# Kernel optimization log

Measured on AMD Instinct MI355X. Metric: run time of the kernel, lower is better.

The kernel has to match this reference:

```python
import jax, jax.numpy as jnp
import numpy as np
from jax import lax

HID = 256
ITERS = 8
KT, KH, KW = 3, 7, 7
NBLK = 3
B_, T_, H_, W_, CIN = 1, 8, 32, 32, 128
NQ = 256


def _layernorm(x, scale, bias, eps=1e-6):
    mu = jnp.mean(x, axis=-1, keepdims=True)
    var = jnp.mean(jnp.square(x - mu), axis=-1, keepdims=True)
    return (x - mu) * lax.rsqrt(var + eps) * scale + bias


def _convssm3d(x, A_kernel, B_kernel):
    # x: (B,T,H,W,C); kernels: (C,kt,kh,kw)
    B, T, H, W, C = x.shape
    A_stable = 0.9 * jnp.tanh(A_kernel)
    tt = (jnp.arange(KT) - KT // 2) % T
    th = (jnp.arange(KH) - KH // 2) % H
    tw = (jnp.arange(KW) - KW // 2) % W
    TT, TH, TW = jnp.meshgrid(tt, th, tw, indexing='ij')

    def to_freq(k):
        pad = jnp.zeros((C, T, H, W), x.dtype).at[:, TT, TH, TW].set(k)
        return jnp.fft.fftn(pad, axes=(1, 2, 3)).transpose(1, 2, 3, 0)[None]  # (1,T,H,W,C)

    A_f = to_freq(A_stable)
    B_f = to_freq(B_kernel)
    Bx_f = B_f * jnp.fft.fftn(x, axes=(1, 2, 3))
    shape = (ITERS,) + x.shape
    a_seq = jnp.broadcast_to(A_f, shape)
    b_seq = jnp.broadcast_to(Bx_f, shape)

    def op(left, right):
        return (left[0] * right[0], right[0] * left[1] + right[1])

    _, h_all = lax.associative_scan(op, (a_seq, b_seq), axis=0)
    return jnp.fft.ifftn(h_all[-1], axes=(1, 2, 3)).real


def setup_inputs() -> dict:
    key = jax.random.key(0)
    ks = jax.random.split(key, 10)
    s = 0.02
    return {
        'video_features': jax.random.normal(ks[0], (B_, T_, H_, W_, CIN), jnp.float32),
        'query_points': jax.random.uniform(ks[1], (B_, NQ, 3), jnp.float32),
        'conv_w': jax.random.normal(ks[2], (CIN, HID), jnp.float32) * s,
        'conv_b': jnp.zeros((HID,), jnp.float32),
        'A_kernels': jax.random.normal(ks[3], (NBLK, HID, KT, KH, KW), jnp.float32) * s,
        'B_kernels': jax.random.normal(ks[4], (NBLK, HID, KT, KH, KW), jnp.float32) * s,
        'ln_scale': jnp.ones((NBLK, HID), jnp.float32),
        'ln_bias': jnp.zeros((NBLK, HID), jnp.float32),
        'mlp_w1': jax.random.normal(ks[5], (NBLK, HID, 4 * HID), jnp.float32) * s,
        'mlp_b1': jnp.zeros((NBLK, 4 * HID), jnp.float32),
        'mlp_w2': jax.random.normal(ks[6], (NBLK, 4 * HID, HID), jnp.float32) * s,
        'mlp_b2': jnp.zeros((NBLK, HID), jnp.float32),
        'traj_w': jax.random.normal(ks[7], (HID, 2), jnp.float32) * s,
        'traj_b': jnp.zeros((2,), jnp.float32),
        'occ_w': jax.random.normal(ks[8], (HID, 1), jnp.float32) * s,
        'occ_b': jnp.zeros((1,), jnp.float32),
    }


def reference(video_features, query_points, conv_w, conv_b, A_kernels, B_kernels,
              ln_scale, ln_bias, mlp_w1, mlp_b1, mlp_w2, mlp_b2,
              traj_w, traj_b, occ_w, occ_b):
    # 1x1x1 conv == channel dense. Query scatter in original is a zeros no-op.
    x = jnp.einsum('bthwc,cd->bthwd', video_features, conv_w) + conv_b
    for i in range(NBLK):
        h = _convssm3d(x, A_kernels[i], B_kernels[i])
        h = _layernorm(h, ln_scale[i], ln_bias[i])
        x = x + h
        m = jax.nn.gelu(x @ mlp_w1[i] + mlp_b1[i])  # approximate gelu (flax default)
        x = x + (m @ mlp_w2[i] + mlp_b2[i])
    feat = jnp.mean(x, axis=(2, 3))  # (B,T,C)
    N = query_points.shape[1]
    fe = jnp.broadcast_to(feat[:, None], (feat.shape[0], N) + feat.shape[1:])  # (B,N,T,C)
    trajectories = fe @ traj_w + traj_b + query_points[..., 1:3][:, :, None, :]  # (B,N,T,2)
    occlusion = jax.nn.sigmoid((fe @ occ_w + occ_b)[..., 0])  # (B,N,T)
    return trajectories, occlusion
```

## Files before the change

### kernel.cpp

```cpp
#include <hip/hip_runtime.h>
#include <hip/hip_bf16.h>
#include <math.h>

#define Tn 8
#define Hn 32
#define Wn 32
#define Pn 8192
#define Cn 256
#define CINn 128
#define NTAP 147
#define PADW 40

typedef short s8v __attribute__((ext_vector_type(8)));
typedef float f4v __attribute__((ext_vector_type(4)));
typedef __hip_bfloat16 bf16;

__device__ __forceinline__ float gelu_f(float v) {
    return 0.5f * v * (1.0f + tanhf(0.7978845608028654f * (v + 0.044715f * v * v * v)));
}

__device__ __forceinline__ void gload_lds16(const bf16* g, bf16* l) {
    __builtin_amdgcn_global_load_lds(
        (const __attribute__((address_space(1))) void*)g,
        (__attribute__((address_space(3))) void*)l, 16, 0, 0);
}

__global__ __launch_bounds__(256) void tcast_all_k(
        const float* __restrict__ convw, const float* __restrict__ w1,
        const float* __restrict__ w2, const float* __restrict__ video,
        bf16* __restrict__ cwT, bf16* __restrict__ w1T, bf16* __restrict__ w2T,
        bf16* __restrict__ vb) {
    const int z = blockIdx.z;
    const int tid = (int)threadIdx.x;
    if (z == 7) {
        const int bx = (int)blockIdx.y * 32 + (int)blockIdx.x;
        const int i = bx * 256 + tid;
        const float4 v = ((const float4*)video)[i];
        vb[i * 4 + 0] = __float2bfloat16(v.x);
        vb[i * 4 + 1] = __float2bfloat16(v.y);
        vb[i * 4 + 2] = __float2bfloat16(v.z);
        vb[i * 4 + 3] = __float2bfloat16(v.w);
        return;
    }
    const float* in;
    bf16* out;
    int R, C;
    if (z == 0)      { in = convw;                          out = cwT;                          R = CINn; C = Cn;   }
    else if (z < 4)  { const int i = z - 1;
                       in = w1 + (size_t)i * Cn * 1024;     out = w1T + (size_t)i * 1024 * Cn;  R = Cn;   C = 1024; }
    else             { const int i = z - 4;
                       in = w2 + (size_t)i * 1024 * Cn;     out = w2T + (size_t)i * Cn * 1024;  R = 1024; C = Cn;   }
    if ((int)blockIdx.x >= (C >> 5) || (int)blockIdx.y >= (R >> 5)) return;

    __shared__ float tile[32][33];
    const int tx = tid & 31, ty = tid >> 5;
    const int rb = blockIdx.y << 5, cb = blockIdx.x << 5;
#pragma unroll
    for (int p = 0; p < 4; ++p)
        tile[ty + p * 8][tx] = in[(size_t)(rb + ty + p * 8) * C + cb + tx];
    __syncthreads();
#pragma unroll
    for (int p = 0; p < 4; ++p)
        out[(size_t)(cb + ty + p * 8) * R + rb + tx] = __float2bfloat16(tile[tx][ty + p * 8]);
}

template <int BN, int MODE>
__global__ __launch_bounds__(256) void gemm_bf16_k(
        const bf16* __restrict__ A, const bf16* __restrict__ Wt,
        const float* __restrict__ bias, float* __restrict__ Cf,
        bf16* __restrict__ Cb, bf16* __restrict__ Cpl, int M, int N, int K) {
    constexpr int BM = 128;
    constexpr int NW = BN / 2;
    constexpr int NF = BN / 32;
    constexpr int ALOADS = (BM * 8) / 256;
    constexpr int BLOADS = (BN * 8) / 256;
    __shared__ s8v As[8 * BM];
    __shared__ s8v Bs[8 * BN];

    const int tid = (int)threadIdx.x;
    const int lane = tid & 63, wid = tid >> 6;
    const int wm = wid & 1, wn = wid >> 1;
    const int l15 = lane & 15, l4 = lane >> 4;
    const int m0 = blockIdx.y * BM;
    const int n0 = blockIdx.x * BN;

    f4v acc[4][NF];
#pragma unroll
    for (int i = 0; i < 4; ++i)
#pragma unroll
        for (int j = 0; j < NF; ++j)
#pragma unroll
            for (int r = 0; r < 4; ++r) acc[i][j][r] = 0.f;

    const bf16* Aptr[ALOADS];
#pragma unroll
    for (int j = 0; j < ALOADS; ++j) {
        const int cid = j * 256 + tid;
        Aptr[j] = A + (size_t)(m0 + (cid & (BM - 1))) * K + (cid / BM) * 8;
    }
    const bf16* Bptr[BLOADS];
#pragma unroll
    for (int j = 0; j < BLOADS; ++j) {
        const int cid = j * 256 + tid;
        Bptr[j] = Wt + (size_t)(n0 + (cid & (BN - 1))) * K + (cid / BN) * 8;
    }

    for (int kb = 0; kb < K; kb += 64) {
#pragma unroll
        for (int j = 0; j < ALOADS; ++j)
            gload_lds16(Aptr[j] + kb, (bf16*)&As[j * 256 + tid]);
#pragma unroll
        for (int j = 0; j < BLOADS; ++j)
            gload_lds16(Bptr[j] + kb, (bf16*)&Bs[j * 256 + tid]);
        __syncthreads();

        s8v af[2][4], bfr[2][NF];
#pragma unroll
        for (int ks = 0; ks < 2; ++ks) {
#pragma unroll
            for (int i = 0; i < 4; ++i)
                af[ks][i] = As[(ks * 4 + l4) * BM + wm * 64 + i * 16 + l15];
#pragma unroll
            for (int j = 0; j < NF; ++j)
                bfr[ks][j] = Bs[(ks * 4 + l4) * BN + wn * NW + j * 16 + l15];
        }
#pragma unroll
        for (int ks = 0; ks < 2; ++ks)
#pragma unroll
            for (int i = 0; i < 4; ++i)
#pragma unroll
                for (int j = 0; j < NF; ++j)
                    acc[i][j] = __builtin_amdgcn_mfma_f32_16x16x32_bf16(
                        af[ks][i], bfr[ks][j], acc[i][j], 0, 0, 0);
        __syncthreads();
    }

#pragma unroll
    for (int i = 0; i < 4; ++i) {
        const int rbase = m0 + wm * 64 + i * 16 + l4 * 4;
#pragma unroll
        for (int j = 0; j < NF; ++j) {
            const int col = n0 + wn * NW + j * 16 + l15;
            const float bv = bias[col];
#pragma unroll
            for (int r = 0; r < 4; ++r) {
                const size_t idx = (size_t)(rbase + r) * N + col;
                float v = acc[i][j][r] + bv;
                if (MODE == 0) Cf[idx] = v;
                if (MODE == 1) Cb[idx] = __float2bfloat16(gelu_f(v));
                if (MODE == 2) { v += Cf[idx]; Cf[idx] = v; }
                if (MODE != 1 && Cpl != nullptr)
                    Cpl[(size_t)col * Pn + rbase + r] = __float2bfloat16(v);
            }
        }
    }
}

#define CLOADS(AS, BS0, BS1, body) do {                                       \
    const int bb_ = (body);                                                   \
    const int kt_ = bb_ < 7 ? 0 : (bb_ < 14 ? 1 : 2);                         \
    const int kh_ = bb_ - kt_ * 7;                                            \
    BS0 = *(const s8v*)&tw[bb_][u0][0];                                       \
    BS1 = *(const s8v*)&tw[bb_][u1][0];                                       \
    _Pragma("unroll")                                                         \
    for (int i_ = 0; i_ < 2; ++i_) {                                          \
        const int tp_ = (tout[i_] - kt_ + 9) & 7;                             \
        const int hin_ = (hl[i_] + 35 - kh_) & 31;                            \
        AS[i_] = *(const s8v*)&pl[(tp_ * 32 + hin_) * PADW + aoff];           \
    }                                                                         \
} while (0)

#define CMFMA(AS, BS0, BS1) do {                                              \
    _Pragma("unroll")                                                         \
    for (int i_ = 0; i_ < 2; ++i_) {                                          \
        acc[i_][0] = __builtin_amdgcn_mfma_f32_16x16x32_bf16(AS[i_], BS0, acc[i_][0], 0, 0, 0); \
        acc[i_][1] = __builtin_amdgcn_mfma_f32_16x16x32_bf16(AS[i_], BS1, acc[i_][1], 0, 0, 0); \
    }                                                                         \
} while (0)

__global__ __launch_bounds__(512) void conv_ssm_k(
        const bf16* __restrict__ xplb,
        const float* __restrict__ Ak,
        const float* __restrict__ Bk,
        float* __restrict__ hpo) {
    __shared__ __align__(16) bf16 Pl[2][256 * PADW];
    __shared__ __align__(16) bf16 Tw[2][21][32][8];
    __shared__ float wtap[2][NTAP];

    const int c = blockIdx.x;
    const int tid = (int)threadIdx.x;
    const int lane = tid & 63, wv = tid >> 6;
    const int l15 = lane & 15, l4 = lane >> 4;

    if (tid < NTAP) {
        wtap[0][tid] = Bk[(size_t)c * NTAP + tid];
        wtap[1][tid] = 0.9f * tanhf(Ak[(size_t)c * NTAP + tid]);
    }
    {
        const s8v* src = (const s8v*)(xplb + (size_t)c * Pn);
#pragma unroll
        for (int j = 0; j < 2; ++j) {
            const int g = j * 512 + tid;
            *(s8v*)&Pl[0][(g >> 2) * PADW + (g & 3) * 8] = src[g];
        }
    }
    __syncthreads();
    for (int e = tid; e < 2 * 21 * 32; e += 512) {
        const int sel = e / 672, rem = e % 672;
        const int body = rem >> 5, u = rem & 31;
        const float* tp = &wtap[sel][body * 7];
        bf16 row[8];
#pragma unroll
        for (int j = 0; j < 8; ++j) {
            const int kw = (u - j) & 31;
            row[j] = __float2bfloat16((kw < 7) ? tp[kw] : 0.f);
        }
        *(s8v*)&Tw[sel][body][u][0] = *(const s8v*)row;
    }

    const int u0 = (l15 - l4 * 8 + 3) & 31;
    const int u1 = (l15 + 16 - l4 * 8 + 3) & 31;
    int tout[2], hl[2];
#pragma unroll
    for (int i = 0; i < 2; ++i) {
        const int f = wv * 2 + i;
        tout[i] = f >> 1;
        hl[i] = ((f & 1) << 4) + l15;
    }
    const int aoff = l4 * 8;

    float hsum[16];
#pragma unroll
    for (int i = 0; i < 16; ++i) hsum[i] = 0.f;
    __syncthreads();

#pragma unroll 1
    for (int it = 0; it < 8; ++it) {
        const bf16* pl = Pl[it & 1];
        bf16* pd = Pl[(it + 1) & 1];
        const bf16 (*tw)[32][8] = Tw[(it == 0) ? 0 : 1];

        f4v acc[2][2];
#pragma unroll
        for (int i = 0; i < 2; ++i)
#pragma unroll
            for (int hf = 0; hf < 2; ++hf)
#pragma unroll
                for (int r = 0; r < 4; ++r) acc[i][hf][r] = 0.f;

        s8v a0[2], a1[2], b00, b01, b10, b11;
        CLOADS(a0, b00, b01, 0);
#pragma unroll 1
        for (int b = 0; b < 20; b += 2) {
            CLOADS(a1, b10, b11, b + 1);
            CMFMA(a0, b00, b01);
            CLOADS(a0, b00, b01, b + 2);
            CMFMA(a1, b10, b11);
        }
        CMFMA(a0, b00, b01);

#pragma unroll
        for (int i = 0; i < 2; ++i) {
            const int rbase = (wv * 2 + i) * 16 + l4 * 4;
#pragma unroll
            for (int hf = 0; hf < 2; ++hf) {
                const int col = l15 + hf * 16;
#pragma unroll
                for (int r = 0; r < 4; ++r) {
                    const float v = acc[i][hf][r];
                    hsum[i * 8 + hf * 4 + r] += v;
                    if (it < 7) pd[(rbase + r) * PADW + col] = __float2bfloat16(v);
                }
            }
        }
        __syncthreads();
    }

    float* o = hpo + (size_t)c * Pn;
#pragma unroll
    for (int i = 0; i < 2; ++i) {
        const int rbase = (wv * 2 + i) * 16 + l4 * 4;
#pragma unroll
        for (int hf = 0; hf < 2; ++hf)
#pragma unroll
            for (int r = 0; r < 4; ++r)
                o[(rbase + r) * 32 + l15 + hf * 16] = hsum[i * 8 + hf * 4 + r];
    }
}

__global__ __launch_bounds__(256) void ln_res_plane_k(
        const float* __restrict__ hpl,
        const float* __restrict__ scale, const float* __restrict__ bias,
        float* __restrict__ x,
        bf16* __restrict__ xb) {
    __shared__ float tile[256][33];
    __shared__ float red[2][32][9];
    __shared__ float mus[32], rss[32];
    const int tid = (int)threadIdx.x;
    const int p0 = blockIdx.x << 5;

    {
        const float* src = hpl + (size_t)tid * Pn + p0;
#pragma unroll
        for (int j = 0; j < 32; j += 4) {
            const float4 v = *(const float4*)(src + j);
            tile[tid][j] = v.x; tile[tid][j + 1] = v.y;
            tile[tid][j + 2] = v.z; tile[tid][j + 3] = v.w;
        }
    }
    __syncthreads();
    {
        const int p = tid & 31, g = tid >> 5;
        float s = 0.f, ss = 0.f;
#pragma unroll
        for (int ci = 0; ci < 32; ++ci) {
            const float v = tile[g * 32 + ci][p];
            s += v; ss += v * v;
        }
        red[0][p][g] = s; red[1][p][g] = ss;
    }
    __syncthreads();
    if (tid < 32) {
        float s = 0.f, ss = 0.f;
#pragma unroll
        for (int g = 0; g < 8; ++g) { s += red[0][tid][g]; ss += red[1][tid][g]; }
        const float mu = s * (1.0f / 256.0f);
        const float var = ss * (1.0f / 256.0f) - mu * mu;
        mus[tid] = mu;
        rss[tid] = rsqrtf(var + 1e-6f);
    }
    __syncthreads();
    {
        const int cch = tid;
        const float sc = scale[cch], bi = bias[cch];
#pragma unroll 4
        for (int j = 0; j < 32; ++j) {
            const size_t idx = (size_t)(p0 + j) * Cn + cch;
            const float normed = (tile[cch][j] - mus[j]) * rss[j] * sc + bi;
            const float xv = x[idx] + normed;
            x[idx] = xv;
            xb[idx] = __float2bfloat16(xv);
        }
    }
}

__global__ void feat_part_k(const float* __restrict__ x, float* __restrict__ part) {
    const int t = blockIdx.x, sgm = blockIdx.y;
    const int c = (int)threadIdx.x;
    float acc = 0.f;
    const float* xp_ = x + ((size_t)t * 1024 + sgm * 128) * Cn + c;
    for (int p = 0; p < 128; ++p) acc += xp_[(size_t)p * Cn];
    part[(t * 8 + sgm) * Cn + c] = acc;
}

__global__ __launch_bounds__(256) void heads_k(
        const float* __restrict__ part, const float* __restrict__ qp,
        const float* __restrict__ traj_w, const float* __restrict__ traj_b,
        const float* __restrict__ occ_w, const float* __restrict__ occ_b,
        float* __restrict__ out) {
    __shared__ float fs[Tn * Cn];
    __shared__ float proj[Tn][3];
    const int tid = (int)threadIdx.x;
    for (int i = tid; i < Tn * Cn; i += 256) {
        const int t = i >> 8, c = i & 255;
        float s = 0.f;
#pragma unroll
        for (int j = 0; j < 8; ++j) s += part[(t * 8 + j) * Cn + c];
        fs[i] = s * (1.0f / 1024.0f);
    }
    __syncthreads();
    if (tid < 24) {
        const int t = tid / 3, j = tid % 3;
        float s = 0.f;
        for (int c = 0; c < Cn; ++c) {
            const float w = (j < 2) ? traj_w[c * 2 + j] : occ_w[c];
            s += fs[t * Cn + c] * w;
        }
        s += (j < 2) ? traj_b[j] : occ_b[0];
        proj[t][j] = s;
    }
    __syncthreads();
    const int n = tid;
#pragma unroll
    for (int t = 0; t < Tn; ++t) {
        out[(n * Tn + t) * 2 + 0] = proj[t][0] + qp[n * 3 + 1];
        out[(n * Tn + t) * 2 + 1] = proj[t][1] + qp[n * 3 + 2];
        out[4096 + n * Tn + t] = 1.0f / (1.0f + expf(-proj[t][2]));
    }
}

extern "C" void kernel_launch(void* const* d_in, const int* in_sizes, int n_in,
                              void* d_out, int out_size, void* d_ws, size_t ws_size,
                              hipStream_t stream) {
    const float* video = (const float*)d_in[0];
    const float* qp    = (const float*)d_in[1];
    const float* convw = (const float*)d_in[2];
    const float* convb = (const float*)d_in[3];
    const float* Ak    = (const float*)d_in[4];
    const float* Bk    = (const float*)d_in[5];
    const float* ln_s  = (const float*)d_in[6];
    const float* ln_b  = (const float*)d_in[7];
    const float* w1    = (const float*)d_in[8];
    const float* b1    = (const float*)d_in[9];
    const float* w2    = (const float*)d_in[10];
    const float* b2    = (const float*)d_in[11];
    const float* tw    = (const float*)d_in[12];
    const float* tb    = (const float*)d_in[13];
    const float* ow    = (const float*)d_in[14];
    const float* ob    = (const float*)d_in[15];

    char* wsb = (char*)d_ws;
    float* x    = (float*)wsb;           wsb += (size_t)Pn * Cn * 4;
    float* hpl  = (float*)wsb;           wsb += (size_t)Pn * Cn * 4;
    bf16*  xplb = (bf16*)wsb;            wsb += (size_t)Pn * Cn * 2;
    bf16*  xb   = (bf16*)wsb;            wsb += (size_t)Pn * Cn * 2;
    bf16*  mb   = (bf16*)wsb;            wsb += (size_t)Pn * 1024 * 2;
    bf16*  vb   = (bf16*)wsb;            wsb += (size_t)Pn * CINn * 2;
    bf16*  cwT  = (bf16*)wsb;            wsb += (size_t)Cn * CINn * 2;
    bf16*  w1T  = (bf16*)wsb;            wsb += (size_t)3 * 1024 * Cn * 2;
    bf16*  w2T  = (bf16*)wsb;            wsb += (size_t)3 * Cn * 1024 * 2;
    float* part = (float*)wsb;           wsb += (size_t)64 * Cn * 4;

    tcast_all_k<<<dim3(32, 32, 8), 256, 0, stream>>>(convw, w1, w2, video,
                                                     cwT, w1T, w2T, vb);

    gemm_bf16_k<32, 0><<<dim3(Cn / 32, Pn / 128), 256, 0, stream>>>(
        vb, cwT, convb, x, nullptr, xplb, Pn, Cn, CINn);

    for (int i = 0; i < 3; ++i) {
        conv_ssm_k<<<Cn, 512, 0, stream>>>(xplb, Ak + (size_t)i * Cn * NTAP,
                                           Bk + (size_t)i * Cn * NTAP, hpl);
        ln_res_plane_k<<<Pn / 32, 256, 0, stream>>>(hpl, ln_s + i * Cn,
                                                    ln_b + i * Cn, x, xb);
        gemm_bf16_k<64, 1><<<dim3(1024 / 64, Pn / 128), 256, 0, stream>>>(
            xb, w1T + (size_t)i * 1024 * Cn, b1 + (size_t)i * 1024, nullptr, mb,
            nullptr, Pn, 1024, Cn);
        gemm_bf16_k<32, 2><<<dim3(Cn / 32, Pn / 128), 256, 0, stream>>>(
            mb, w2T + (size_t)i * Cn * 1024, b2 + (size_t)i * Cn, x, nullptr,
            (i < 2) ? xplb : nullptr, Pn, Cn, 1024);
    }

    feat_part_k<<<dim3(Tn, 8), 256, 0, stream>>>(x, part);
    heads_k<<<1, 256, 0, stream>>>(part, qp, tw, tb, ow, ob, (float*)d_out);
}
```

Baseline: 314.0 us.

## Fuse layernorm residual and both MLP GEMMs into one per-tile kernel

```diff
diff --git a/kernel.cpp b/kernel.cpp
--- a/kernel.cpp
+++ b/kernel.cpp
@@ -10,6 +10,8 @@
 #define CINn 128
 #define NTAP 147
 #define PADW 40
+#define XBP 264
+#define MLP_ 1032
 
 typedef short s8v __attribute__((ext_vector_type(8)));
 typedef float f4v __attribute__((ext_vector_type(4)));
@@ -156,6 +158,169 @@
     }
 }
 
+__global__ __launch_bounds__(512) void mlp_fused_k(
+        const float* __restrict__ hpl,
+        const float* __restrict__ lns, const float* __restrict__ lnb,
+        float* __restrict__ x,
+        const bf16* __restrict__ w1T,
+        const float* __restrict__ b1,
+        const bf16* __restrict__ w2T,
+        const float* __restrict__ b2,
+        bf16* __restrict__ xplb) {
+    __shared__ union {
+        float tileA[256][33];
+        bf16  m_lds[32 * MLP_];
+    } U;
+    __shared__ __align__(16) s8v stage[4096];
+    __shared__ __align__(16) bf16 xb_lds[32 * XBP];
+    __shared__ float red[2][32][17];
+    __shared__ float mus[32], rss[32];
+
+    const int tid = (int)threadIdx.x;
+    const int p0 = (int)blockIdx.x * 32;
+    const int lane = tid & 63, wid = tid >> 6;
+    const int l15 = lane & 15, l4 = lane >> 4;
+
+    const int c = tid & 255, half = tid >> 8;
+    {
+        const float* src = hpl + (size_t)c * Pn + p0 + half * 16;
+#pragma unroll
+        for (int j = 0; j < 16; j += 4) {
+            const float4 v = *(const float4*)(src + j);
+            U.tileA[c][half * 16 + j]     = v.x;
+            U.tileA[c][half * 16 + j + 1] = v.y;
+            U.tileA[c][half * 16 + j + 2] = v.z;
+            U.tileA[c][half * 16 + j + 3] = v.w;
+        }
+    }
+    __syncthreads();
+    {
+        const int p = tid & 31, g = tid >> 5;
+        float s = 0.f, ss = 0.f;
+#pragma unroll
+        for (int ci = 0; ci < 16; ++ci) {
+            const float v = U.tileA[g * 16 + ci][p];
+            s += v; ss += v * v;
+        }
+        red[0][p][g] = s; red[1][p][g] = ss;
+    }
+    __syncthreads();
+    if (tid < 32) {
+        float s = 0.f, ss = 0.f;
+#pragma unroll
+        for (int g = 0; g < 16; ++g) { s += red[0][tid][g]; ss += red[1][tid][g]; }
+        const float mu = s * (1.0f / 256.0f);
+        const float var = ss * (1.0f / 256.0f) - mu * mu;
+        mus[tid] = mu;
+        rss[tid] = rsqrtf(var + 1e-6f);
+    }
+    __syncthreads();
+    {
+        const float sc = lns[c], bi = lnb[c];
+#pragma unroll
+        for (int j = 0; j < 16; ++j) {
+            const int p = half * 16 + j;
+            const size_t idx = (size_t)(p0 + p) * Cn + c;
+            const float nm = (U.tileA[c][p] - mus[p]) * rss[p] * sc + bi;
+            const float xv = x[idx] + nm;
+            x[idx] = xv;
+            xb_lds[p * XBP + c] = __float2bfloat16(xv);
+        }
+    }
+    __syncthreads();
+
+#pragma unroll 1
+    for (int nc = 0; nc < 8; ++nc) {
+#pragma unroll
+        for (int j = 0; j < 8; ++j) {
+            const int cid = j * 512 + tid;
+            const int nl = cid & 127, k8 = cid >> 7;
+            gload_lds16(w1T + (size_t)(nc * 128 + nl) * 256 + k8 * 8,
+                        (bf16*)&stage[cid]);
+        }
+        __syncthreads();
+
+        f4v a1[2];
+#pragma unroll
+        for (int i = 0; i < 2; ++i)
+#pragma unroll
+            for (int r = 0; r < 4; ++r) a1[i][r] = 0.f;
+#pragma unroll
+        for (int ks = 0; ks < 8; ++ks) {
+            const s8v bfr = stage[(ks * 4 + l4) * 128 + wid * 16 + l15];
+#pragma unroll
+            for (int i = 0; i < 2; ++i) {
+                const s8v af = *(const s8v*)&xb_lds[(i * 16 + l15) * XBP + ks * 32 + l4 * 8];
+                a1[i] = __builtin_amdgcn_mfma_f32_16x16x32_bf16(af, bfr, a1[i], 0, 0, 0);
+            }
+        }
+        const int colb = nc * 128 + wid * 16 + l15;
+        const float bv = b1[colb];
+#pragma unroll
+        for (int i = 0; i < 2; ++i) {
+            const int row = i * 16 + l4 * 4;
+#pragma unroll
+            for (int r = 0; r < 4; ++r)
+                U.m_lds[(row + r) * MLP_ + colb] = __float2bfloat16(gelu_f(a1[i][r] + bv));
+        }
+        __syncthreads();
+    }
+
+    f4v a2[2][2];
+#pragma unroll
+    for (int i = 0; i < 2; ++i)
+#pragma unroll
+        for (int j = 0; j < 2; ++j)
+#pragma unroll
+            for (int r = 0; r < 4; ++r) a2[i][j][r] = 0.f;
+
+#pragma unroll 1
+    for (int kc = 0; kc < 8; ++kc) {
+#pragma unroll
+        for (int j = 0; j < 8; ++j) {
+            const int cid = j * 512 + tid;
+            const int nl = cid & 255, k8 = cid >> 8;
+            gload_lds16(w2T + (size_t)nl * 1024 + kc * 128 + k8 * 8,
+                        (bf16*)&stage[cid]);
+        }
+        __syncthreads();
+#pragma unroll
+        for (int ks = 0; ks < 4; ++ks) {
+            s8v b2f[2];
+#pragma unroll
+            for (int j = 0; j < 2; ++j)
+                b2f[j] = stage[(ks * 4 + l4) * 256 + wid * 32 + j * 16 + l15];
+#pragma unroll
+            for (int i = 0; i < 2; ++i) {
+                const s8v af = *(const s8v*)&U.m_lds[(i * 16 + l15) * MLP_ +
+                                                     kc * 128 + ks * 32 + l4 * 8];
+#pragma unroll
+                for (int j = 0; j < 2; ++j)
+                    a2[i][j] = __builtin_amdgcn_mfma_f32_16x16x32_bf16(af, b2f[j], a2[i][j], 0, 0, 0);
+            }
+        }
+        __syncthreads();
+    }
+
+#pragma unroll
+    for (int i = 0; i < 2; ++i) {
+#pragma unroll
+        for (int j = 0; j < 2; ++j) {
+            const int col = wid * 32 + j * 16 + l15;
+            const float bv = b2[col];
+#pragma unroll
+            for (int r = 0; r < 4; ++r) {
+                const int row = i * 16 + l4 * 4 + r;
+                const size_t idx = (size_t)(p0 + row) * Cn + col;
+                const float v = x[idx] + a2[i][j][r] + bv;
+                x[idx] = v;
+                if (xplb != nullptr)
+                    xplb[(size_t)col * Pn + p0 + row] = __float2bfloat16(v);
+            }
+        }
+    }
+}
+
 #define CLOADS(AS, BS0, BS1, body) do {                                       \
     const int bb_ = (body);                                                   \
     const int kt_ = bb_ < 7 ? 0 : (bb_ < 14 ? 1 : 2);                         \
@@ -285,62 +450,6 @@
 #pragma unroll
             for (int r = 0; r < 4; ++r)
                 o[(rbase + r) * 32 + l15 + hf * 16] = hsum[i * 8 + hf * 4 + r];
-    }
-}
-
-__global__ __launch_bounds__(256) void ln_res_plane_k(
-        const float* __restrict__ hpl,
-        const float* __restrict__ scale, const float* __restrict__ bias,
-        float* __restrict__ x,
-        bf16* __restrict__ xb) {
-    __shared__ float tile[256][33];
-    __shared__ float red[2][32][9];
-    __shared__ float mus[32], rss[32];
-    const int tid = (int)threadIdx.x;
-    const int p0 = blockIdx.x << 5;
-
-    {
-        const float* src = hpl + (size_t)tid * Pn + p0;
-#pragma unroll
-        for (int j = 0; j < 32; j += 4) {
-            const float4 v = *(const float4*)(src + j);
-            tile[tid][j] = v.x; tile[tid][j + 1] = v.y;
-            tile[tid][j + 2] = v.z; tile[tid][j + 3] = v.w;
-        }
-    }
-    __syncthreads();
-    {
-        const int p = tid & 31, g = tid >> 5;
-        float s = 0.f, ss = 0.f;
-#pragma unroll
-        for (int ci = 0; ci < 32; ++ci) {
-            const float v = tile[g * 32 + ci][p];
-            s += v; ss += v * v;
-        }
-        red[0][p][g] = s; red[1][p][g] = ss;
-    }
-    __syncthreads();
-    if (tid < 32) {
-        float s = 0.f, ss = 0.f;
-#pragma unroll
-        for (int g = 0; g < 8; ++g) { s += red[0][tid][g]; ss += red[1][tid][g]; }
-        const float mu = s * (1.0f / 256.0f);
-        const float var = ss * (1.0f / 256.0f) - mu * mu;
-        mus[tid] = mu;
-        rss[tid] = rsqrtf(var + 1e-6f);
-    }
-    __syncthreads();
-    {
-        const int cch = tid;
-        const float sc = scale[cch], bi = bias[cch];
-#pragma unroll 4
-        for (int j = 0; j < 32; ++j) {
-            const size_t idx = (size_t)(p0 + j) * Cn + cch;
-            const float normed = (tile[cch][j] - mus[j]) * rss[j] * sc + bi;
-            const float xv = x[idx] + normed;
-            x[idx] = xv;
-            xb[idx] = __float2bfloat16(xv);
-        }
     }
 }
 
@@ -413,8 +522,6 @@
     float* x    = (float*)wsb;           wsb += (size_t)Pn * Cn * 4;
     float* hpl  = (float*)wsb;           wsb += (size_t)Pn * Cn * 4;
     bf16*  xplb = (bf16*)wsb;            wsb += (size_t)Pn * Cn * 2;
-    bf16*  xb   = (bf16*)wsb;            wsb += (size_t)Pn * Cn * 2;
-    bf16*  mb   = (bf16*)wsb;            wsb += (size_t)Pn * 1024 * 2;
     bf16*  vb   = (bf16*)wsb;            wsb += (size_t)Pn * CINn * 2;
     bf16*  cwT  = (bf16*)wsb;            wsb += (size_t)Cn * CINn * 2;
     bf16*  w1T  = (bf16*)wsb;            wsb += (size_t)3 * 1024 * Cn * 2;
@@ -430,14 +537,11 @@
     for (int i = 0; i < 3; ++i) {
         conv_ssm_k<<<Cn, 512, 0, stream>>>(xplb, Ak + (size_t)i * Cn * NTAP,
                                            Bk + (size_t)i * Cn * NTAP, hpl);
-        ln_res_plane_k<<<Pn / 32, 256, 0, stream>>>(hpl, ln_s + i * Cn,
-                                                    ln_b + i * Cn, x, xb);
-        gemm_bf16_k<64, 1><<<dim3(1024 / 64, Pn / 128), 256, 0, stream>>>(
-            xb, w1T + (size_t)i * 1024 * Cn, b1 + (size_t)i * 1024, nullptr, mb,
-            nullptr, Pn, 1024, Cn);
-        gemm_bf16_k<32, 2><<<dim3(Cn / 32, Pn / 128), 256, 0, stream>>>(
-            mb, w2T + (size_t)i * Cn * 1024, b2 + (size_t)i * Cn, x, nullptr,
-            (i < 2) ? xplb : nullptr, Pn, Cn, 1024);
+        mlp_fused_k<<<Pn / 32, 512, 0, stream>>>(
+            hpl, ln_s + i * Cn, ln_b + i * Cn, x,
+            w1T + (size_t)i * 1024 * Cn, b1 + (size_t)i * 1024,
+            w2T + (size_t)i * Cn * 1024, b2 + (size_t)i * Cn,
+            (i < 2) ? xplb : nullptr);
     }
 
     feat_part_k<<<dim3(Tn, 8), 256, 0, stream>>>(x, part);
```

After: 334.0 us. 1.06x slower.

## Store GEMM operands in tile-contiguous chunked layout for coalesced LDS loads

Applied to the files above, without the earlier changes.

```diff
diff --git a/kernel.cpp b/kernel.cpp
--- a/kernel.cpp
+++ b/kernel.cpp
@@ -23,6 +23,15 @@
     __builtin_amdgcn_global_load_lds(
         (const __attribute__((address_space(1))) void*)g,
         (__attribute__((address_space(3))) void*)l, 16, 0, 0);
+}
+
+__device__ __forceinline__ size_t caddrA(int K, int m, int k) {
+    return ((size_t)(m >> 7) * (K >> 6) + (k >> 6)) * 8192 +
+           (size_t)((((k >> 3) & 7) * 128 + (m & 127)) * 8 + (k & 7));
+}
+__device__ __forceinline__ size_t caddrB(int K, int BN, int n, int k) {
+    return ((size_t)(n / BN) * (K >> 6) + (k >> 6)) * (size_t)(BN * 64) +
+           (size_t)((((k >> 3) & 7) * BN + (n % BN)) * 8 + (k & 7));
 }
 
 __global__ __launch_bounds__(256) void tcast_all_k(
@@ -35,21 +44,23 @@
     if (z == 7) {
         const int bx = (int)blockIdx.y * 32 + (int)blockIdx.x;
         const int i = bx * 256 + tid;
+        const int p = i >> 5, c0 = (i & 31) * 4;
         const float4 v = ((const float4*)video)[i];
-        vb[i * 4 + 0] = __float2bfloat16(v.x);
-        vb[i * 4 + 1] = __float2bfloat16(v.y);
-        vb[i * 4 + 2] = __float2bfloat16(v.z);
-        vb[i * 4 + 3] = __float2bfloat16(v.w);
+        const size_t a0 = caddrA(CINn, p, c0);
+        vb[a0 + 0] = __float2bfloat16(v.x);
+        vb[a0 + 1] = __float2bfloat16(v.y);
+        vb[a0 + 2] = __float2bfloat16(v.z);
+        vb[a0 + 3] = __float2bfloat16(v.w);
         return;
     }
     const float* in;
     bf16* out;
-    int R, C;
-    if (z == 0)      { in = convw;                          out = cwT;                          R = CINn; C = Cn;   }
+    int R, C, bn;
+    if (z == 0)      { in = convw;                       out = cwT;                          R = CINn; C = Cn;   bn = 32; }
     else if (z < 4)  { const int i = z - 1;
-                       in = w1 + (size_t)i * Cn * 1024;     out = w1T + (size_t)i * 1024 * Cn;  R = Cn;   C = 1024; }
+                       in = w1 + (size_t)i * Cn * 1024;  out = w1T + (size_t)i * 1024 * Cn;  R = Cn;   C = 1024; bn = 64; }
     else             { const int i = z - 4;
-                       in = w2 + (size_t)i * 1024 * Cn;     out = w2T + (size_t)i * Cn * 1024;  R = 1024; C = Cn;   }
+                       in = w2 + (size_t)i * 1024 * Cn;  out = w2T + (size_t)i * Cn * 1024;  R = 1024; C = Cn;   bn = 32; }
     if ((int)blockIdx.x >= (C >> 5) || (int)blockIdx.y >= (R >> 5)) return;
 
     __shared__ float tile[32][33];
@@ -61,10 +72,10 @@
     __syncthreads();
 #pragma unroll
     for (int p = 0; p < 4; ++p)
-        out[(size_t)(cb + ty + p * 8) * R + rb + tx] = __float2bfloat16(tile[tx][ty + p * 8]);
-}
-
-template <int BN, int MODE>
+        out[caddrB(R, bn, cb + ty + p * 8, rb + tx)] = __float2bfloat16(tile[tx][ty + p * 8]);
+}
+
+template <int BN, int MODE, int ACH>
 __global__ __launch_bounds__(256) void gemm_bf16_k(
         const bf16* __restrict__ A, const bf16* __restrict__ Wt,
         const float* __restrict__ bias, float* __restrict__ Cf,
@@ -72,7 +83,7 @@
     constexpr int BM = 128;
     constexpr int NW = BN / 2;
     constexpr int NF = BN / 32;
-    constexpr int ALOADS = (BM * 8) / 256;
+    constexpr int ALOADS = 4;
     constexpr int BLOADS = (BN * 8) / 256;
     __shared__ s8v As[8 * BM];
     __shared__ s8v Bs[8 * BN];
@@ -92,26 +103,33 @@
 #pragma unroll
             for (int r = 0; r < 4; ++r) acc[i][j][r] = 0.f;
 
-    const bf16* Aptr[ALOADS];
-#pragma unroll
-    for (int j = 0; j < ALOADS; ++j) {
-        const int cid = j * 256 + tid;
-        Aptr[j] = A + (size_t)(m0 + (cid & (BM - 1))) * K + (cid / BM) * 8;
-    }
-    const bf16* Bptr[BLOADS];
-#pragma unroll
-    for (int j = 0; j < BLOADS; ++j) {
-        const int cid = j * 256 + tid;
-        Bptr[j] = Wt + (size_t)(n0 + (cid & (BN - 1))) * K + (cid / BN) * 8;
-    }
-
-    for (int kb = 0; kb < K; kb += 64) {
-#pragma unroll
-        for (int j = 0; j < ALOADS; ++j)
-            gload_lds16(Aptr[j] + kb, (bf16*)&As[j * 256 + tid]);
+    const bf16* Ach = A + ((size_t)(m0 >> 7) * (K >> 6)) * 8192;
+    const bf16* Aln[ALOADS];
+    if (ACH == 0) {
+#pragma unroll
+        for (int j = 0; j < ALOADS; ++j) {
+            const int cid = j * 256 + tid;
+            Aln[j] = A + (size_t)(m0 + (cid & (BM - 1))) * K + (cid / BM) * 8;
+        }
+    }
+    const bf16* Bch = Wt + ((size_t)(n0 / BN) * (K >> 6)) * (size_t)(BN * 64);
+
+    int kc = 0;
+    for (int kb = 0; kb < K; kb += 64, ++kc) {
+        if (ACH == 1) {
+#pragma unroll
+            for (int j = 0; j < ALOADS; ++j)
+                gload_lds16(Ach + (size_t)kc * 8192 + (j * 256 + tid) * 8,
+                            (bf16*)&As[j * 256 + tid]);
+        } else {
+#pragma unroll
+            for (int j = 0; j < ALOADS; ++j)
+                gload_lds16(Aln[j] + kb, (bf16*)&As[j * 256 + tid]);
+        }
 #pragma unroll
         for (int j = 0; j < BLOADS; ++j)
-            gload_lds16(Bptr[j] + kb, (bf16*)&Bs[j * 256 + tid]);
+            gload_lds16(Bch + (size_t)kc * (BN * 64) + (j * 256 + tid) * 8,
+                        (bf16*)&Bs[j * 256 + tid]);
         __syncthreads();
 
         s8v af[2][4], bfr[2][NF];
@@ -147,7 +165,7 @@
                 const size_t idx = (size_t)(rbase + r) * N + col;
                 float v = acc[i][j][r] + bv;
                 if (MODE == 0) Cf[idx] = v;
-                if (MODE == 1) Cb[idx] = __float2bfloat16(gelu_f(v));
+                if (MODE == 1) Cb[caddrA(N, rbase + r, col)] = __float2bfloat16(gelu_f(v));
                 if (MODE == 2) { v += Cf[idx]; Cf[idx] = v; }
                 if (MODE != 1 && Cpl != nullptr)
                     Cpl[(size_t)col * Pn + rbase + r] = __float2bfloat16(v);
@@ -424,7 +442,7 @@
     tcast_all_k<<<dim3(32, 32, 8), 256, 0, stream>>>(convw, w1, w2, video,
                                                      cwT, w1T, w2T, vb);
 
-    gemm_bf16_k<32, 0><<<dim3(Cn / 32, Pn / 128), 256, 0, stream>>>(
+    gemm_bf16_k<32, 0, 1><<<dim3(Cn / 32, Pn / 128), 256, 0, stream>>>(
         vb, cwT, convb, x, nullptr, xplb, Pn, Cn, CINn);
 
     for (int i = 0; i < 3; ++i) {
@@ -432,10 +450,10 @@
                                            Bk + (size_t)i * Cn * NTAP, hpl);
         ln_res_plane_k<<<Pn / 32, 256, 0, stream>>>(hpl, ln_s + i * Cn,
                                                     ln_b + i * Cn, x, xb);
-        gemm_bf16_k<64, 1><<<dim3(1024 / 64, Pn / 128), 256, 0, stream>>>(
+        gemm_bf16_k<64, 1, 0><<<dim3(1024 / 64, Pn / 128), 256, 0, stream>>>(
             xb, w1T + (size_t)i * 1024 * Cn, b1 + (size_t)i * 1024, nullptr, mb,
             nullptr, Pn, 1024, Cn);
-        gemm_bf16_k<32, 2><<<dim3(Cn / 32, Pn / 128), 256, 0, stream>>>(
+        gemm_bf16_k<32, 2, 1><<<dim3(Cn / 32, Pn / 128), 256, 0, stream>>>(
             mb, w2T + (size_t)i * Cn * 1024, b2 + (size_t)i * Cn, x, nullptr,
             (i < 2) ? xplb : nullptr, Pn, Cn, 1024);
     }
```

After: 293.8 us, median of 2. 1.07x faster.
